# Performance work log

Measured on AMD Instinct MI355X. Metric: run time of the kernel, lower is better.

Reference implementation:

```python
import jax, jax.numpy as jnp
import numpy as np

N, E, B = 60000, 360000, 64        # nodes, edges, graphs
IN_DIM, HID, L, NCLS = 256, 512, 3, 1000
EPS = 1e-5                          # BatchNorm1d eps


def setup_inputs() -> dict:
    key = jax.random.key(0)
    ks = jax.random.split(key, 10)
    s = 0.05
    x = jax.random.normal(ks[0], (N, IN_DIM), dtype=jnp.float32)
    edge_index = jax.random.randint(ks[1], (2, E), 0, N, dtype=jnp.int32)
    batch = jnp.sort(jax.random.randint(ks[2], (N,), 0, B, dtype=jnp.int32))
    W_embed = jax.random.normal(ks[3], (IN_DIM, HID), dtype=jnp.float32) * s
    # per-block params (all 3 blocks have identical shapes -> stacked on axis 0)
    W1 = jax.random.normal(ks[4], (L, 2 * HID, HID), dtype=jnp.float32) * s
    b1 = jnp.zeros((L, HID), jnp.float32)
    g1 = jnp.ones((L, HID), jnp.float32)
    be1 = jnp.zeros((L, HID), jnp.float32)
    W2 = jax.random.normal(ks[5], (L, 2 * HID, HID), dtype=jnp.float32) * s
    b2 = jnp.zeros((L, HID), jnp.float32)
    g2 = jnp.ones((L, HID), jnp.float32)
    be2 = jnp.zeros((L, HID), jnp.float32)
    W_att = jax.random.normal(ks[6], (HID, 1), dtype=jnp.float32) * s
    W_read = jax.random.normal(ks[7], (HID, NCLS), dtype=jnp.float32) * s
    return dict(x=x, edge_index=edge_index, batch=batch, W_embed=W_embed,
                W1=W1, b1=b1, g1=g1, be1=be1, W2=W2, b2=b2, g2=g2, be2=be2,
                W_att=W_att, W_read=W_read)


def _segment_mean(vals, idx, num):
    s = jax.ops.segment_sum(vals, idx, num_segments=num)
    c = jax.ops.segment_sum(jnp.ones((vals.shape[0], 1), vals.dtype), idx, num_segments=num)
    return s / jnp.maximum(c, 1.0)


def _bn(h, g, b):  # BatchNorm1d, training-mode batch statistics (biased var)
    m = h.mean(0)
    v = jnp.mean((h - m) ** 2, axis=0)
    return (h - m) * jax.lax.rsqrt(v + EPS) * g + b


def _sage(h, src, dst, W, b):
    # MySAGEConv (position=False -> message = x_j), aggr='mean', concat=True, L2 normalize
    aggr = _segment_mean(h[src], dst, h.shape[0])          # [N, d] mean of neighbor msgs
    out = jnp.concatenate([h, aggr], axis=-1) @ W + b      # [N, 2d] @ [2d, d]
    norm = jnp.linalg.norm(out, axis=-1, keepdims=True)
    return out / jnp.maximum(norm, 1e-12)                  # F.normalize(p=2)


def reference(x, edge_index, batch, W_embed, W1, b1, g1, be1,
              W2, b2, g2, be2, W_att, W_read):
    src, dst = edge_index[0], edge_index[1]
    h = x @ W_embed
    for l in range(L):  # MySAGEConvBlock, gcn_num=2, has_linear_in_block=False
        identity = h
        out = jax.nn.relu(_bn(_sage(h, src, dst, W1[l], b1[l]), g1[l], be1[l]))
        out = jax.nn.relu(_bn(_sage(out, src, dst, W2[l], b2[l]), g2[l], be2[l]))
        h = out + identity  # residual (dims match)
    # AttentionClass
    att = jax.nn.sigmoid(h @ W_att)           # [N, 1]
    hx = (att * h + h) * 0.5
    hg = _segment_mean(hx, batch, B)          # global mean pool per graph
    return hg @ W_read                        # [B, 1000] logits
```

## Files before the change

kernel.cpp:

```cpp
#include <hip/hip_runtime.h>
#include <math.h>

#define N_NODES 60000
#define N_EDGES 360000
#define N_GRAPH 64
#define HID 512
#define NCLS 1000
#define BN_EPS 1e-5f
#define NS ((size_t)N_NODES * HID)
#define NB 235
#define STRIPS 469

typedef __bf16 bf16x8 __attribute__((ext_vector_type(8)));
typedef float f32x4 __attribute__((ext_vector_type(4)));

static __device__ __forceinline__ unsigned short f2bf(float f) {
  unsigned u = __float_as_uint(f);
  unsigned r = (u + 0x7fffu + ((u >> 16) & 1u)) >> 16;
  return (unsigned short)r;
}
static __device__ __forceinline__ float bfLo(unsigned u) { return __uint_as_float(u << 16); }
static __device__ __forceinline__ float bfHi(unsigned u) { return __uint_as_float(u & 0xffff0000u); }
static __device__ __forceinline__ unsigned packbf(float a, float b) {
  return (unsigned)f2bf(a) | ((unsigned)f2bf(b) << 16);
}

__global__ void write_sentinel(float* out, float v) { out[0] = v; }

__global__ __launch_bounds__(256) void cvt_bf16(const float* __restrict__ X,
                                                unsigned short* __restrict__ Y,
                                                long n4) {
  long i = (long)blockIdx.x * 256 + threadIdx.x;
  if (i >= n4) return;
  float4 f = *(const float4*)(X + i * 4);
  uint2 o;
  o.x = packbf(f.x, f.y);
  o.y = packbf(f.z, f.w);
  *(uint2*)(Y + i * 4) = o;
}

__global__ __launch_bounds__(256) void wtrans(const float* __restrict__ W,
                                              unsigned short* __restrict__ Wt,
                                              int K, int N,
                                              size_t strideW, size_t strideWt) {
  __shared__ float sh[32][33];
  W += (size_t)blockIdx.z * strideW;
  Wt += (size_t)blockIdx.z * strideWt;
  int kt = blockIdx.x * 32, nt = blockIdx.y * 32;
  int tx = threadIdx.x & 31, ty = threadIdx.x >> 5;
#pragma unroll
  for (int i = 0; i < 4; ++i)
    sh[ty + i * 8][tx] = W[(size_t)(kt + ty + i * 8) * N + nt + tx];
  __syncthreads();
#pragma unroll
  for (int i = 0; i < 4; ++i)
    Wt[(size_t)(nt + ty + i * 8) * K + kt + tx] = f2bf(sh[tx][ty + i * 8]);
}

__global__ __launch_bounds__(256) void count_deg(const int* __restrict__ dst,
                                                 int* __restrict__ deg, int E) {
  int e = blockIdx.x * 256 + threadIdx.x;
  if (e < E) atomicAdd(&deg[dst[e]], 1);
}

__global__ __launch_bounds__(256) void make_invdeg(const int* __restrict__ deg,
                                                   float* __restrict__ inv, int n) {
  int i = blockIdx.x * 256 + threadIdx.x;
  if (i < n) inv[i] = 1.0f / fmaxf((float)deg[i], 1.0f);
}

__global__ __launch_bounds__(256) void scan_part(const int* __restrict__ deg,
                                                 int* __restrict__ bsum, int n) {
  __shared__ int sh[256];
  int i = blockIdx.x * 256 + threadIdx.x;
  sh[threadIdx.x] = (i < n) ? deg[i] : 0;
  __syncthreads();
  for (int off = 128; off; off >>= 1) {
    if (threadIdx.x < off) sh[threadIdx.x] += sh[threadIdx.x + off];
    __syncthreads();
  }
  if (threadIdx.x == 0) bsum[blockIdx.x] = sh[0];
}

__global__ __launch_bounds__(256) void scan_bsums(int* __restrict__ bsum, int nb) {
  __shared__ int sh[256];
  int t = threadIdx.x;
  int v = (t < nb) ? bsum[t] : 0;
  sh[t] = v;
  __syncthreads();
  for (int off = 1; off < 256; off <<= 1) {
    int u = (t >= off) ? sh[t - off] : 0;
    __syncthreads();
    sh[t] += u;
    __syncthreads();
  }
  if (t < nb) bsum[t] = sh[t] - v;
}

__global__ __launch_bounds__(256) void scan_final(const int* __restrict__ deg,
                                                  const int* __restrict__ bsum,
                                                  int* __restrict__ rowptr, int n) {
  __shared__ int sh[256];
  int t = threadIdx.x;
  int i = blockIdx.x * 256 + t;
  int v = (i < n) ? deg[i] : 0;
  sh[t] = v;
  __syncthreads();
  for (int off = 1; off < 256; off <<= 1) {
    int u = (t >= off) ? sh[t - off] : 0;
    __syncthreads();
    sh[t] += u;
    __syncthreads();
  }
  if (i < n) rowptr[i + 1] = bsum[blockIdx.x] + sh[t];
  if (i == 0) rowptr[0] = 0;
}

__global__ __launch_bounds__(256) void fill_csr(const int* __restrict__ src,
                                                const int* __restrict__ dst,
                                                const int* __restrict__ rowptr,
                                                int* __restrict__ fillc,
                                                int* __restrict__ esrc, int E) {
  int e = blockIdx.x * 256 + threadIdx.x;
  if (e < E) {
    int d = dst[e];
    int pos = rowptr[d] + atomicAdd(&fillc[d], 1);
    esrc[pos] = src[e];
  }
}

__global__ __launch_bounds__(256) void bcount(const int* __restrict__ batch,
                                              float* __restrict__ bcnt, int n) {
  __shared__ int h[N_GRAPH];
  if (threadIdx.x < N_GRAPH) h[threadIdx.x] = 0;
  __syncthreads();
  int i = blockIdx.x * 256 + threadIdx.x;
  if (i < n) atomicAdd(&h[batch[i]], 1);
  __syncthreads();
  if (threadIdx.x < N_GRAPH && h[threadIdx.x])
    atomicAdd(&bcnt[threadIdx.x], (float)h[threadIdx.x]);
}

#define GEMM_BODY(Xb, ldx, Wtb, ldw, bias_p, outp, KDIM)                        \
  unsigned short* As = (unsigned short*)smem;                                   \
  unsigned short* Bs = (unsigned short*)(smem + 8192);                          \
  typedef unsigned short CsRow[136];                                            \
  CsRow* Cs = (CsRow*)smem;                                                     \
  const int wv = tid >> 6, lane = tid & 63;                                     \
  const int wm = (wv >> 1) * 64, wn = (wv & 1) * 64;                            \
  const int lm = lane & 15, quad = lane >> 4;                                   \
  const int grow = lane & 15, gseg = (lane >> 4) * 8;                           \
  f32x4 zero; zero[0] = 0.f; zero[1] = 0.f; zero[2] = 0.f; zero[3] = 0.f;       \
  f32x4 acc[4][4];                                                              \
  _Pragma("unroll") for (int i = 0; i < 4; ++i)                                 \
    _Pragma("unroll") for (int j = 0; j < 4; ++j) acc[i][j] = zero;             \
  for (int kt = 0; kt < (KDIM); kt += 32) {                                     \
    __syncthreads();                                                            \
    _Pragma("unroll") for (int r = 0; r < 2; ++r) {                             \
      int chunk = wv + r * 4;                                                   \
      int row = chunk * 16 + grow;                                              \
      const unsigned short* ga = (Xb) + (size_t)(bm + row) * (ldx) + kt + gseg; \
      const unsigned short* gb = (Wtb) + (size_t)(bn + row) * (ldw) + kt + gseg;\
      __builtin_amdgcn_global_load_lds(                                         \
          (const __attribute__((address_space(1))) unsigned int*)ga,            \
          (__attribute__((address_space(3))) unsigned int*)(As + chunk * 512),  \
          16, 0, 0);                                                            \
      __builtin_amdgcn_global_load_lds(                                         \
          (const __attribute__((address_space(1))) unsigned int*)gb,            \
          (__attribute__((address_space(3))) unsigned int*)(Bs + chunk * 512),  \
          16, 0, 0);                                                            \
    }                                                                           \
    __syncthreads();                                                            \
    bf16x8 af[4], bfr[4];                                                       \
    _Pragma("unroll") for (int i = 0; i < 4; ++i)                               \
      af[i] = *(const bf16x8*)(As + (wm / 16 + i) * 512 + lane * 8);            \
    _Pragma("unroll") for (int j = 0; j < 4; ++j)                               \
      bfr[j] = *(const bf16x8*)(Bs + (wn / 16 + j) * 512 + lane * 8);           \
    _Pragma("unroll") for (int i = 0; i < 4; ++i)                               \
      _Pragma("unroll") for (int j = 0; j < 4; ++j)                             \
        acc[i][j] = __builtin_amdgcn_mfma_f32_16x16x32_bf16(af[i], bfr[j],      \
                                                            acc[i][j], 0, 0, 0);\
  }                                                                             \
  const int qr = quad * 4;                                                      \
  const int rl = tid >> 4, seg = (tid & 15) * 8;                                \
  _Pragma("unroll") for (int p = 0; p < 2; ++p) {                               \
    __syncthreads();                                                            \
    if ((wv >> 1) == p) {                                                       \
      _Pragma("unroll") for (int j = 0; j < 4; ++j) {                           \
        int col = wn + j * 16 + lm;                                             \
        float bvv = (bias_p) ? (bias_p)[bn + col] : 0.f;                        \
        _Pragma("unroll") for (int i = 0; i < 4; ++i)                           \
          _Pragma("unroll") for (int r = 0; r < 4; ++r)                         \
            Cs[i * 16 + qr + r][col] = f2bf(acc[i][j][r] + bvv);                \
      }                                                                         \
    }                                                                           \
    __syncthreads();                                                            \
    _Pragma("unroll") for (int pass = 0; pass < 4; ++pass) {                    \
      int row = bm + p * 64 + pass * 16 + rl;                                   \
      if (row < M)                                                              \
        *(uint4*)((outp) + (size_t)row * 512 + bn + seg) =                      \
            *(const uint4*)(&Cs[pass * 16 + rl][seg]);                          \
    }                                                                           \
  }

__global__ __launch_bounds__(256) void gemm_glds(
    const unsigned short* __restrict__ Xb, int ldx, int K,
    const unsigned short* __restrict__ Wt, int ldw,
    const float* __restrict__ bias,
    unsigned short* __restrict__ outB, int M) {
  __shared__ __align__(16) unsigned char smem[17408];
  const int tid = threadIdx.x;
  const int L = blockIdx.x;
  const int xcd = L & 7, li = L >> 3;
  const int strip = xcd * 59 + (li >> 2);
  if (strip >= STRIPS) return;
  const int bm = strip * 128;
  const int bn = (li & 3) * 128;
  GEMM_BODY(Xb, ldx, Wt, ldw, bias, outB, K)
}

__global__ __launch_bounds__(256) void gemm_dual(
    const unsigned short* __restrict__ Xb, int ldx,
    const unsigned short* __restrict__ Wt,
    const float* __restrict__ biasA,
    unsigned short* __restrict__ outA, unsigned short* __restrict__ outBf,
    int M) {
  __shared__ __align__(16) unsigned char smem[17408];
  const int tid = threadIdx.x;
  const int L = blockIdx.x;
  const int xcd = L & 7, li = L >> 3;
  const int strip = xcd * 59 + (li >> 3);
  if (strip >= STRIPS) return;
  const int cb = li & 7;
  const int bm = strip * 128;
  const int bn = (cb & 3) * 128;
  const unsigned short* Wtb = Wt + (cb < 4 ? 0 : 512);
  const float* bias = (cb < 4) ? biasA : nullptr;
  unsigned short* outp = (cb < 4) ? outA : outBf;
  GEMM_BODY(Xb, ldx, Wtb, 1024, bias, outp, 512)
}

__global__ __launch_bounds__(512) void gemm_strip(
    const unsigned short* __restrict__ Xb, int ldx,
    const unsigned short* __restrict__ Wt, int ldw,
    const float* __restrict__ bias,
    unsigned short* __restrict__ outB, int M) {
  __shared__ __align__(16) unsigned short As[64][40];
  const int tid = threadIdx.x;
  const int bm = blockIdx.x * 64;
  const int wv = tid >> 6, lane = tid & 63;
  const int lm = lane & 15, quad = lane >> 4, lk = quad * 8;
  const int cb = wv * 64;
  const int arow = tid >> 3, aseg = (tid & 7) * 4;

  f32x4 zero;
  zero[0] = 0.f; zero[1] = 0.f; zero[2] = 0.f; zero[3] = 0.f;
  f32x4 acc[4][4];
#pragma unroll
  for (int i = 0; i < 4; ++i)
#pragma unroll
    for (int j = 0; j < 4; ++j) acc[i][j] = zero;

  for (int kt = 0; kt < 512; kt += 32) {
    uint2 av = make_uint2(0, 0);
    int gr = bm + arow;
    if (gr < M) av = *(const uint2*)(Xb + (size_t)gr * ldx + kt + aseg);
    bf16x8 bfr[4];
#pragma unroll
    for (int j = 0; j < 4; ++j)
      bfr[j] = *(const bf16x8*)(Wt + (size_t)(cb + j * 16 + lm) * ldw + kt + lk);
    __syncthreads();
    *(uint2*)(&As[arow][aseg]) = av;
    __syncthreads();
    bf16x8 af[4];
#pragma unroll
    for (int i = 0; i < 4; ++i) af[i] = *(const bf16x8*)(&As[i * 16 + lm][lk]);
#pragma unroll
    for (int i = 0; i < 4; ++i)
#pragma unroll
      for (int j = 0; j < 4; ++j)
        acc[i][j] = __builtin_amdgcn_mfma_f32_16x16x32_bf16(af[i], bfr[j], acc[i][j], 0, 0, 0);
  }

  const int qr = quad * 4;
#pragma unroll
  for (int j = 0; j < 4; ++j) {
    int col = cb + j * 16 + lm;
    float bvv = bias ? bias[col] : 0.f;
#pragma unroll
    for (int i = 0; i < 4; ++i) {
      int rbase = bm + i * 16 + qr;
#pragma unroll
      for (int r = 0; r < 4; ++r) {
        int row = rbase + r;
        if (row < M) outB[(size_t)row * 512 + col] = f2bf(acc[i][j][r] + bvv);
      }
    }
  }
}

__global__ __launch_bounds__(256) void aggr_norm(
    unsigned short* __restrict__ Ya, const unsigned short* __restrict__ Yb,
    const int* __restrict__ rowptr, const int* __restrict__ esrc,
    const float* __restrict__ invdeg, int M) {
  int d = blockIdx.x * 4 + (threadIdx.x >> 6);
  int lane = threadIdx.x & 63;
  if (d >= M) return;
  float acc[8] = {0.f, 0.f, 0.f, 0.f, 0.f, 0.f, 0.f, 0.f};
  int beg = rowptr[d], end = rowptr[d + 1];
  for (int e = beg; e < end; ++e) {
    int s = esrc[e];
    uint4 u = *(const uint4*)(Yb + (size_t)s * 512 + lane * 8);
    acc[0] += bfLo(u.x); acc[1] += bfHi(u.x);
    acc[2] += bfLo(u.y); acc[3] += bfHi(u.y);
    acc[4] += bfLo(u.z); acc[5] += bfHi(u.z);
    acc[6] += bfLo(u.w); acc[7] += bfHi(u.w);
  }
  float iv = invdeg[d];
  uint4 a = *(const uint4*)(Ya + (size_t)d * 512 + lane * 8);
  float r0 = bfLo(a.x) + iv * acc[0], r1 = bfHi(a.x) + iv * acc[1];
  float r2 = bfLo(a.y) + iv * acc[2], r3 = bfHi(a.y) + iv * acc[3];
  float r4 = bfLo(a.z) + iv * acc[4], r5 = bfHi(a.z) + iv * acc[5];
  float r6 = bfLo(a.w) + iv * acc[6], r7 = bfHi(a.w) + iv * acc[7];
  float ss = r0 * r0 + r1 * r1 + r2 * r2 + r3 * r3
           + r4 * r4 + r5 * r5 + r6 * r6 + r7 * r7;
#pragma unroll
  for (int o = 32; o; o >>= 1) ss += __shfl_xor(ss, o, 64);
  float inv = 1.0f / fmaxf(sqrtf(ss), 1e-12f);
  uint4 o4;
  o4.x = packbf(r0 * inv, r1 * inv);
  o4.y = packbf(r2 * inv, r3 * inv);
  o4.z = packbf(r4 * inv, r5 * inv);
  o4.w = packbf(r6 * inv, r7 * inv);
  *(uint4*)(Ya + (size_t)d * 512 + lane * 8) = o4;
}

__global__ __launch_bounds__(256) void bn_stats(const unsigned short* __restrict__ T,
                                                int M, float* __restrict__ sums) {
  const int t = threadIdx.x;
  int r0 = blockIdx.x * 32;
  int rend = min(r0 + 32, M);
  float s0 = 0.f, q0 = 0.f, s1 = 0.f, q1 = 0.f;
  for (int r = r0; r < rend; ++r) {
    float a = __uint_as_float((unsigned)T[(size_t)r * 512 + t] << 16);
    float b = __uint_as_float((unsigned)T[(size_t)r * 512 + t + 256] << 16);
    s0 += a; q0 += a * a; s1 += b; q1 += b * b;
  }
  atomicAdd(&sums[t], s0);
  atomicAdd(&sums[t + 256], s1);
  atomicAdd(&sums[512 + t], q0);
  atomicAdd(&sums[512 + t + 256], q1);
}

__global__ __launch_bounds__(256) void bn_apply(const unsigned short* __restrict__ U,
                                                unsigned short* __restrict__ H,
                                                const float* __restrict__ sums,
                                                const float* __restrict__ g,
                                                const float* __restrict__ be,
                                                int M, int residual) {
  size_t i4 = (size_t)blockIdx.x * 256 + threadIdx.x;
  if (i4 >= NS / 8) return;
  int c = (int)((i4 * 8) & 511);
  float invM = 1.0f / (float)M;
  uint4 u4 = ((const uint4*)U)[i4];
  uint4 h4;
  if (residual) h4 = ((const uint4*)H)[i4];
  unsigned uin[4] = {u4.x, u4.y, u4.z, u4.w};
  unsigned hin[4] = {h4.x, h4.y, h4.z, h4.w};
  unsigned outv[4];
#pragma unroll
  for (int k = 0; k < 4; ++k) {
    int c0 = c + k * 2;
    float m0 = sums[c0] * invM, m1 = sums[c0 + 1] * invM;
    float v0 = sums[512 + c0] * invM - m0 * m0;
    float v1 = sums[512 + c0 + 1] * invM - m1 * m1;
    float k0 = rsqrtf(v0 + BN_EPS) * g[c0], k1 = rsqrtf(v1 + BN_EPS) * g[c0 + 1];
    float x0 = fmaxf((bfLo(uin[k]) - m0) * k0 + be[c0], 0.f);
    float x1 = fmaxf((bfHi(uin[k]) - m1) * k1 + be[c0 + 1], 0.f);
    if (residual) { x0 += bfLo(hin[k]); x1 += bfHi(hin[k]); }
    outv[k] = packbf(x0, x1);
  }
  uint4 o4 = make_uint4(outv[0], outv[1], outv[2], outv[3]);
  ((uint4*)H)[i4] = o4;
}

#define NPB 64
__global__ __launch_bounds__(256) void att_pool2(const unsigned short* __restrict__ H,
                                                 const int* __restrict__ batch,
                                                 const float* __restrict__ Watt,
                                                 float* __restrict__ hg, int M) {
  __shared__ float fsh[NPB];
  __shared__ int bsh[NPB];
  const int tid = threadIdx.x;
  const int base = blockIdx.x * NPB;
  if (tid < NPB) bsh[tid] = (base + tid < M) ? batch[base + tid] : -1;
  const int wv = tid >> 6, lane = tid & 63;
  float4 wa0 = *(const float4*)(Watt + lane * 8);
  float4 wa1 = *(const float4*)(Watt + lane * 8 + 4);
  __syncthreads();
  for (int i = wv; i < NPB; i += 4) {
    int node = base + i;
    float dot = 0.f;
    if (node < M) {
      uint4 u = *(const uint4*)(H + (size_t)node * 512 + lane * 8);
      dot = bfLo(u.x) * wa0.x + bfHi(u.x) * wa0.y
          + bfLo(u.y) * wa0.z + bfHi(u.y) * wa0.w
          + bfLo(u.z) * wa1.x + bfHi(u.z) * wa1.y
          + bfLo(u.w) * wa1.z + bfHi(u.w) * wa1.w;
    }
#pragma unroll
    for (int o = 32; o; o >>= 1) dot += __shfl_xor(dot, o, 64);
    if (lane == 0) fsh[i] = 0.5f * (1.0f + 1.0f / (1.0f + expf(-dot)));
  }
  __syncthreads();
  float a0 = 0.f, a1 = 0.f;
  int cur = bsh[0];
  for (int i = 0; i < NPB; ++i) {
    int node = base + i;
    if (node >= M) break;
    int b = bsh[i];
    if (b != cur) {
      atomicAdd(&hg[(size_t)cur * 512 + tid * 2], a0);
      atomicAdd(&hg[(size_t)cur * 512 + tid * 2 + 1], a1);
      a0 = a1 = 0.f;
      cur = b;
    }
    unsigned u = *(const unsigned*)(H + (size_t)node * 512 + tid * 2);
    float f = fsh[i];
    a0 += bfLo(u) * f;
    a1 += bfHi(u) * f;
  }
  if (cur >= 0) {
    atomicAdd(&hg[(size_t)cur * 512 + tid * 2], a0);
    atomicAdd(&hg[(size_t)cur * 512 + tid * 2 + 1], a1);
  }
}

__global__ __launch_bounds__(256) void readout(const float* __restrict__ hg,
                                               const float* __restrict__ bcnt,
                                               const float* __restrict__ Wr,
                                               float* __restrict__ out) {
  __shared__ float sh[HID];
  int g = blockIdx.x;
  int n = blockIdx.y * 256 + threadIdx.x;
  float inv = 1.0f / fmaxf(bcnt[g], 1.0f);
  for (int k = threadIdx.x; k < HID; k += 256) sh[k] = hg[(size_t)g * HID + k] * inv;
  __syncthreads();
  if (n < NCLS) {
    float acc = 0.f;
    for (int k = 0; k < HID; ++k) acc += sh[k] * Wr[(size_t)k * NCLS + n];
    out[(size_t)g * NCLS + n] = acc;
  }
}

extern "C" void kernel_launch(void* const* d_in, const int* in_sizes, int n_in,
                              void* d_out, int out_size, void* d_ws, size_t ws_size,
                              hipStream_t stream) {
  const float* x       = (const float*)d_in[0];
  const int*   ei      = (const int*)d_in[1];
  const int*   batch   = (const int*)d_in[2];
  const float* W_embed = (const float*)d_in[3];
  const float* W1      = (const float*)d_in[4];
  const float* b1      = (const float*)d_in[5];
  const float* g1      = (const float*)d_in[6];
  const float* be1     = (const float*)d_in[7];
  const float* W2      = (const float*)d_in[8];
  const float* b2      = (const float*)d_in[9];
  const float* g2      = (const float*)d_in[10];
  const float* be2     = (const float*)d_in[11];
  const float* Watt    = (const float*)d_in[12];
  const float* Wread   = (const float*)d_in[13];
  float* out = (float*)d_out;

  const int* srcIdx = ei;
  const int* dstIdx = ei + N_EDGES;

  char* p = (char*)d_ws;
  unsigned short* B0 = (unsigned short*)p; p += NS * 2;
  unsigned short* B1 = (unsigned short*)p; p += NS * 2;
  unsigned short* B2 = (unsigned short*)p; p += NS * 2;
  unsigned short* WtE = (unsigned short*)p; p += (size_t)512 * 256 * 2;
  unsigned short* Wt1 = (unsigned short*)p; p += (size_t)3 * 512 * 1024 * 2;
  unsigned short* Wt2 = (unsigned short*)p; p += (size_t)3 * 512 * 1024 * 2;
  float* hg     = (float*)p; p += (size_t)N_GRAPH * HID * 4;
  float* sums   = (float*)p; p += 1024 * 4;
  float* invdeg = (float*)p; p += (size_t)N_NODES * 4;
  float* bcnt   = (float*)p; p += 256;
  int* deg      = (int*)p;   p += (size_t)N_NODES * 4;
  int* fillc    = (int*)p;   p += (size_t)N_NODES * 4;
  int* esrc     = (int*)p;   p += (size_t)N_EDGES * 4;
  int* rowptr   = (int*)p;   p += (size_t)(N_NODES + 1) * 4;
  int* bsum     = (int*)p;   p += (size_t)NB * 4;
  size_t need = (size_t)(p - (char*)d_ws);
  if (ws_size < need) {
    write_sentinel<<<1, 1, 0, stream>>>(out, (float)need);
    return;
  }
  unsigned short* B3 = nullptr;
  if (ws_size >= need + NS * 2) B3 = (unsigned short*)((char*)d_ws + need);

  wtrans<<<dim3(8, 16, 1), 256, 0, stream>>>(W_embed, WtE, 256, 512, 0, 0);
  wtrans<<<dim3(32, 16, 3), 256, 0, stream>>>(W1, Wt1, 1024, 512,
                                              (size_t)1024 * 512, (size_t)512 * 1024);
  wtrans<<<dim3(32, 16, 3), 256, 0, stream>>>(W2, Wt2, 1024, 512,
                                              (size_t)1024 * 512, (size_t)512 * 1024);

  hipMemsetAsync(deg, 0, N_NODES * sizeof(int), stream);
  hipMemsetAsync(fillc, 0, N_NODES * sizeof(int), stream);
  count_deg<<<(N_EDGES + 255) / 256, 256, 0, stream>>>(dstIdx, deg, N_EDGES);
  make_invdeg<<<(N_NODES + 255) / 256, 256, 0, stream>>>(deg, invdeg, N_NODES);
  scan_part<<<NB, 256, 0, stream>>>(deg, bsum, N_NODES);
  scan_bsums<<<1, 256, 0, stream>>>(bsum, NB);
  scan_final<<<NB, 256, 0, stream>>>(deg, bsum, rowptr, N_NODES);
  fill_csr<<<(N_EDGES + 255) / 256, 256, 0, stream>>>(srcIdx, dstIdx, rowptr, fillc,
                                                      esrc, N_EDGES);

  const int g1grid = 8 * 59 * 4;
  const int g2grid = 8 * 59 * 8;
  const int sgrid  = (N_NODES + 63) / 64;
  const int ngrid  = (N_NODES + 3) / 4;
  const int bgrid  = (N_NODES + 31) / 32;
  const int egrid  = (int)((NS / 8 + 255) / 256);

  cvt_bf16<<<(int)(((size_t)N_NODES * 64 + 255) / 256), 256, 0, stream>>>(
      x, B1, (long)N_NODES * 64);
  gemm_glds<<<g1grid, 256, 0, stream>>>(B1, 256, 256, WtE, 256, nullptr, B0, N_NODES);

  for (int l = 0; l < 3; ++l) {
    const unsigned short* Wt1l = Wt1 + (size_t)l * 512 * 1024;
    const unsigned short* Wt2l = Wt2 + (size_t)l * 512 * 1024;
    gemm_dual<<<g2grid, 256, 0, stream>>>(B0, 512, Wt1l, b1 + l * 512, B1, B2, N_NODES);
    aggr_norm<<<ngrid, 256, 0, stream>>>(B1, B2, rowptr, esrc, invdeg, N_NODES);
    hipMemsetAsync(sums, 0, 1024 * sizeof(float), stream);
    bn_stats<<<bgrid, 256, 0, stream>>>(B1, N_NODES, sums);
    bn_apply<<<egrid, 256, 0, stream>>>(B1, B1, sums, g1 + l * 512,
                                        be1 + l * 512, N_NODES, 0);
    unsigned short* Ya2 = B3 ? B3 : B1;
    if (B3) {
      gemm_dual<<<g2grid, 256, 0, stream>>>(B1, 512, Wt2l, b2 + l * 512, B3, B2,
                                            N_NODES);
    } else {
      gemm_glds<<<g1grid, 256, 0, stream>>>(B1, 512, 512, Wt2l + 512, 1024,
                                            nullptr, B2, N_NODES);
      gemm_strip<<<sgrid, 512, 0, stream>>>(B1, 512, Wt2l, 1024,
                                            b2 + l * 512, B1, N_NODES);
    }
    aggr_norm<<<ngrid, 256, 0, stream>>>(Ya2, B2, rowptr, esrc, invdeg, N_NODES);
    hipMemsetAsync(sums, 0, 1024 * sizeof(float), stream);
    bn_stats<<<bgrid, 256, 0, stream>>>(Ya2, N_NODES, sums);
    bn_apply<<<egrid, 256, 0, stream>>>(Ya2, B0, sums, g2 + l * 512,
                                        be2 + l * 512, N_NODES, 1);
  }

  hipMemsetAsync(hg, 0, (size_t)N_GRAPH * HID * sizeof(float), stream);
  hipMemsetAsync(bcnt, 0, N_GRAPH * sizeof(float), stream);
  bcount<<<NB, 256, 0, stream>>>(batch, bcnt, N_NODES);
  att_pool2<<<(N_NODES + NPB - 1) / NPB, 256, 0, stream>>>(B0, batch, Watt, hg, N_NODES);
  readout<<<dim3(N_GRAPH, 4), 256, 0, stream>>>(hg, bcnt, Wread, out);
}
```

Before: 1.963 ms.

## Double-buffer GEMM LDS tiles and unroll neighbor gather by four

The shared GEMM body now keeps two LDS stages and issues the next k-tile's global_load_lds before computing on the current one, so there is one barrier per iteration instead of two. The goal is to overlap global-to-LDS transfer with MFMA work. LDS per block grows to 32 KB, which can lower occupancy. Separately, the neighbor aggregation loop gathers four source rows at a time to raise memory-level parallelism in the irregular gather.

```diff
diff --git a/kernel.cpp b/kernel.cpp
--- a/kernel.cpp
+++ b/kernel.cpp
@@ -141,9 +141,28 @@
     atomicAdd(&bcnt[threadIdx.x], (float)h[threadIdx.x]);
 }
 
+#define GEMM_STAGE(Xb, ldx, Wtb, ldw, ktv, sel)                                 \
+  {                                                                             \
+    unsigned short* dA = base + (sel) * 8192;                                   \
+    unsigned short* dB = dA + 4096;                                             \
+    _Pragma("unroll") for (int r = 0; r < 2; ++r) {                             \
+      int chunk = wv + r * 4;                                                   \
+      int row = chunk * 16 + grow;                                              \
+      const unsigned short* ga = (Xb) + (size_t)(bm + row) * (ldx) + (ktv) + gseg; \
+      const unsigned short* gb = (Wtb) + (size_t)(bn + row) * (ldw) + (ktv) + gseg;\
+      __builtin_amdgcn_global_load_lds(                                         \
+          (const __attribute__((address_space(1))) unsigned int*)ga,            \
+          (__attribute__((address_space(3))) unsigned int*)(dA + chunk * 512),  \
+          16, 0, 0);                                                            \
+      __builtin_amdgcn_global_load_lds(                                         \
+          (const __attribute__((address_space(1))) unsigned int*)gb,            \
+          (__attribute__((address_space(3))) unsigned int*)(dB + chunk * 512),  \
+          16, 0, 0);                                                            \
+    }                                                                           \
+  }
+
 #define GEMM_BODY(Xb, ldx, Wtb, ldw, bias_p, outp, KDIM)                        \
-  unsigned short* As = (unsigned short*)smem;                                   \
-  unsigned short* Bs = (unsigned short*)(smem + 8192);                          \
+  unsigned short* base = (unsigned short*)smem;                                 \
   typedef unsigned short CsRow[136];                                            \
   CsRow* Cs = (CsRow*)smem;                                                     \
   const int wv = tid >> 6, lane = tid & 63;                                     \
@@ -154,28 +173,18 @@
   f32x4 acc[4][4];                                                              \
   _Pragma("unroll") for (int i = 0; i < 4; ++i)                                 \
     _Pragma("unroll") for (int j = 0; j < 4; ++j) acc[i][j] = zero;             \
-  for (int kt = 0; kt < (KDIM); kt += 32) {                                     \
+  const int T = (KDIM) / 32;                                                    \
+  GEMM_STAGE(Xb, ldx, Wtb, ldw, 0, 0)                                           \
+  for (int t = 0; t < T; ++t) {                                                 \
     __syncthreads();                                                            \
-    _Pragma("unroll") for (int r = 0; r < 2; ++r) {                             \
-      int chunk = wv + r * 4;                                                   \
-      int row = chunk * 16 + grow;                                              \
-      const unsigned short* ga = (Xb) + (size_t)(bm + row) * (ldx) + kt + gseg; \
-      const unsigned short* gb = (Wtb) + (size_t)(bn + row) * (ldw) + kt + gseg;\
-      __builtin_amdgcn_global_load_lds(                                         \
-          (const __attribute__((address_space(1))) unsigned int*)ga,            \
-          (__attribute__((address_space(3))) unsigned int*)(As + chunk * 512),  \
-          16, 0, 0);                                                            \
-      __builtin_amdgcn_global_load_lds(                                         \
-          (const __attribute__((address_space(1))) unsigned int*)gb,            \
-          (__attribute__((address_space(3))) unsigned int*)(Bs + chunk * 512),  \
-          16, 0, 0);                                                            \
-    }                                                                           \
-    __syncthreads();                                                            \
+    if (t + 1 < T) GEMM_STAGE(Xb, ldx, Wtb, ldw, (t + 1) * 32, (t + 1) & 1)     \
+    const unsigned short* AsC = base + (t & 1) * 8192;                          \
+    const unsigned short* BsC = AsC + 4096;                                     \
     bf16x8 af[4], bfr[4];                                                       \
     _Pragma("unroll") for (int i = 0; i < 4; ++i)                               \
-      af[i] = *(const bf16x8*)(As + (wm / 16 + i) * 512 + lane * 8);            \
+      af[i] = *(const bf16x8*)(AsC + (wm / 16 + i) * 512 + lane * 8);           \
     _Pragma("unroll") for (int j = 0; j < 4; ++j)                               \
-      bfr[j] = *(const bf16x8*)(Bs + (wn / 16 + j) * 512 + lane * 8);           \
+      bfr[j] = *(const bf16x8*)(BsC + (wn / 16 + j) * 512 + lane * 8);          \
     _Pragma("unroll") for (int i = 0; i < 4; ++i)                               \
       _Pragma("unroll") for (int j = 0; j < 4; ++j)                             \
         acc[i][j] = __builtin_amdgcn_mfma_f32_16x16x32_bf16(af[i], bfr[j],      \
@@ -208,7 +217,7 @@
     const unsigned short* __restrict__ Wt, int ldw,
     const float* __restrict__ bias,
     unsigned short* __restrict__ outB, int M) {
-  __shared__ __align__(16) unsigned char smem[17408];
+  __shared__ __align__(16) unsigned char smem[32768];
   const int tid = threadIdx.x;
   const int L = blockIdx.x;
   const int xcd = L & 7, li = L >> 3;
@@ -225,7 +234,7 @@
     const float* __restrict__ biasA,
     unsigned short* __restrict__ outA, unsigned short* __restrict__ outBf,
     int M) {
-  __shared__ __align__(16) unsigned char smem[17408];
+  __shared__ __align__(16) unsigned char smem[32768];
   const int tid = threadIdx.x;
   const int L = blockIdx.x;
   const int xcd = L & 7, li = L >> 3;
@@ -308,7 +317,23 @@
   if (d >= M) return;
   float acc[8] = {0.f, 0.f, 0.f, 0.f, 0.f, 0.f, 0.f, 0.f};
   int beg = rowptr[d], end = rowptr[d + 1];
-  for (int e = beg; e < end; ++e) {
+  int e = beg;
+  for (; e + 4 <= end; e += 4) {
+    int s0 = esrc[e], s1 = esrc[e + 1], s2 = esrc[e + 2], s3 = esrc[e + 3];
+    uint4 u0 = *(const uint4*)(Yb + (size_t)s0 * 512 + lane * 8);
+    uint4 u1 = *(const uint4*)(Yb + (size_t)s1 * 512 + lane * 8);
+    uint4 u2 = *(const uint4*)(Yb + (size_t)s2 * 512 + lane * 8);
+    uint4 u3 = *(const uint4*)(Yb + (size_t)s3 * 512 + lane * 8);
+    acc[0] += bfLo(u0.x) + bfLo(u1.x) + bfLo(u2.x) + bfLo(u3.x);
+    acc[1] += bfHi(u0.x) + bfHi(u1.x) + bfHi(u2.x) + bfHi(u3.x);
+    acc[2] += bfLo(u0.y) + bfLo(u1.y) + bfLo(u2.y) + bfLo(u3.y);
+    acc[3] += bfHi(u0.y) + bfHi(u1.y) + bfHi(u2.y) + bfHi(u3.y);
+    acc[4] += bfLo(u0.z) + bfLo(u1.z) + bfLo(u2.z) + bfLo(u3.z);
+    acc[5] += bfHi(u0.z) + bfHi(u1.z) + bfHi(u2.z) + bfHi(u3.z);
+    acc[6] += bfLo(u0.w) + bfLo(u1.w) + bfLo(u2.w) + bfLo(u3.w);
+    acc[7] += bfHi(u0.w) + bfHi(u1.w) + bfHi(u2.w) + bfHi(u3.w);
+  }
+  for (; e < end; ++e) {
     int s = esrc[e];
     uint4 u = *(const uint4*)(Yb + (size_t)s * 512 + lane * 8);
     acc[0] += bfLo(u.x); acc[1] += bfHi(u.x);
```

Measured after the change: 1.943 ms. About the same (-1.0%).
